# Kernel optimization log

Measured on AMD Instinct MI355X. Metric: run time of the kernel, lower is better.

The kernel has to match this reference:

```python
import jax, jax.numpy as jnp
import numpy as np

B, T, D, H, E, K = 8, 4096, 768, 3072, 4, 2


def setup_inputs() -> dict:
    key = jax.random.key(0)
    ks = jax.random.split(key, 7)
    s = 0.02
    return {
        "x": jax.random.normal(ks[0], (B, T, D), dtype=jnp.float32),
        "router_w": jax.random.normal(ks[1], (D, E), dtype=jnp.float32) * s,
        "router_b": jnp.zeros((E,), dtype=jnp.float32),
        "W1": jax.random.normal(ks[2], (E, D, H), dtype=jnp.float32) * s,
        "b1": jnp.zeros((E, H), dtype=jnp.float32),
        "W2": jax.random.normal(ks[3], (E, H, D), dtype=jnp.float32) * s,
        "b2": jnp.zeros((E, D), dtype=jnp.float32),
    }


def reference(x, router_w, router_b, W1, b1, W2, b2):
    # Router: softmax over experts, then top-k selection.
    logits = jnp.einsum('btd,de->bte', x, router_w) + router_b        # [B,T,E]
    probs = jax.nn.softmax(logits, axis=-1)                           # [B,T,E]
    topk_probs, topk_idx = jax.lax.top_k(probs, K)                    # [B,T,K]

    # Per-expert combine weight: sum of top-k probs assigned to expert e.
    onehot = jax.nn.one_hot(topk_idx, E, dtype=x.dtype)               # [B,T,K,E]
    w = jnp.einsum('btk,btke->bte', topk_probs, onehot)               # [B,T,E]

    # Expert FFNs (exact-erf GELU matches torch F.gelu default).
    out = jnp.zeros_like(x)
    for e in range(E):
        h = jax.nn.gelu(jnp.einsum('btd,dh->bth', x, W1[e]) + b1[e], approximate=False)
        y = jnp.einsum('bth,hd->btd', h, W2[e]) + b2[e]
        out = out + w[..., e:e + 1] * y

    # Load-balance loss: expert assignment counts (non-differentiable, from int idx).
    counts = onehot.sum(axis=(0, 1, 2))                               # [E]
    token_fraction = counts / counts.sum()
    router_prob_mean = probs.mean(axis=(0, 1))                        # [E]
    load_balance_loss = E * jnp.sum(router_prob_mean * token_fraction)
    return out, load_balance_loss
```

## Files before the change

### kernel.cpp

```cpp
#include <hip/hip_runtime.h>
#include <hip/hip_bf16.h>
#include <hip/hip_fp16.h>

#define N_TOK 32768
#define D_DIM 768
#define H_DIM 3072
#define E_NUM 4
#define MT_PAD (N_TOK + 512)

#define TILE_E 4096

typedef _Float16 f16_t;
typedef _Float16 f16x8 __attribute__((ext_vector_type(8)));
typedef float f32x4 __attribute__((ext_vector_type(4)));

__device__ __forceinline__ f16_t f2h(float f) { return (f16_t)f; }

__device__ __forceinline__ void gload16(const void* g, void* l) {
  __builtin_amdgcn_global_load_lds(
      (const __attribute__((address_space(1))) void*)g,
      (__attribute__((address_space(3))) void*)l,
      16, 0, 0);
}

__device__ __forceinline__ void pipe_barrier() {
  asm volatile("" ::: "memory");
  __builtin_amdgcn_sched_barrier(0);
  __builtin_amdgcn_s_barrier();
  __builtin_amdgcn_sched_barrier(0);
  asm volatile("" ::: "memory");
}

__device__ __forceinline__ int xcd_swizzle(int f, int nwg) {
  const int q = nwg >> 3, r = nwg & 7;
  const int xcd = f & 7, pos = f >> 3;
  return (xcd < r ? xcd * (q + 1) : r * (q + 1) + (xcd - r) * q) + pos;
}


__global__ __launch_bounds__(256) void fill_kernel(unsigned* __restrict__ idx0,
                                                   unsigned* __restrict__ idx1) {
  const int t = blockIdx.x * 256 + threadIdx.x;
  for (int i = t; i < MT_PAD; i += gridDim.x * 256) {
    idx0[i] = 0xFFFFFFFFu;
    idx1[i] = 0xFFFFFFFFu;
  }
}

__global__ __launch_bounds__(256) void transform_kernel(
    const float* __restrict__ in, f16_t* __restrict__ outT,
    int R, int C, int NT, int KT) {
  __shared__ float tile[32][33];
  const int ez = blockIdx.z;
  in += (size_t)ez * R * C;
  const int c0 = blockIdx.x * 32, r0 = blockIdx.y * 32;
  const int tc = threadIdx.x & 31, tr = threadIdx.x >> 5;
#pragma unroll
  for (int i = 0; i < 32; i += 8)
    tile[tr + i][tc] = in[(size_t)(r0 + tr + i) * C + c0 + tc];
  __syncthreads();
  const int kt = r0 >> 5, g = tc >> 3, kk = tc & 7;
#pragma unroll
  for (int i = 0; i < 32; i += 8) {
    const int n = c0 + tr + i;
    const int nt = n >> 7, rl = n & 127;
    outT[(((size_t)(ez * NT + nt)) * KT + kt) * TILE_E + g * 1024 + rl * 8 + kk]
        = f2h(tile[tc][tr + i]);
  }
}

__global__ __launch_bounds__(256) void router_kernel(
    const float* __restrict__ x, const float* __restrict__ rw, const float* __restrict__ rb,
    float* __restrict__ wcomb, int* __restrict__ pairinfo,
    float* __restrict__ psum_part, int* __restrict__ cnt_part,
    int* __restrict__ cnt0_part, int* __restrict__ cnt1_part) {
  __shared__ float rwT[E_NUM][D_DIM];
  __shared__ float prW[4][E_NUM];
  __shared__ int   cnW[4][E_NUM];
  __shared__ int   cn0W[4][E_NUM];
  __shared__ int   cn1W[4][E_NUM];
  const int tid = threadIdx.x;
  for (int i = tid; i < D_DIM * E_NUM; i += 256) {
    int k = i >> 2, e = i & 3;
    rwT[e][k] = rw[i];
  }
  __syncthreads();
  const int lane = tid & 63, wv_ = tid >> 6;
  float pacc[E_NUM] = {0.f, 0.f, 0.f, 0.f};
  int   cacc[E_NUM] = {0, 0, 0, 0};
  int   c0acc[E_NUM] = {0, 0, 0, 0};
  int   c1acc[E_NUM] = {0, 0, 0, 0};
  const int tok0 = blockIdx.x * 32 + wv_ * 8;
  for (int t = 0; t < 8; ++t) {
    const int m = tok0 + t;
    const float* xr = x + (size_t)m * D_DIM;
    float s0 = 0.f, s1 = 0.f, s2 = 0.f, s3 = 0.f;
#pragma unroll
    for (int i = 0; i < D_DIM / 64; ++i) {
      int k = lane + i * 64;
      float xv = xr[k];
      s0 += xv * rwT[0][k]; s1 += xv * rwT[1][k];
      s2 += xv * rwT[2][k]; s3 += xv * rwT[3][k];
    }
#pragma unroll
    for (int off = 32; off >= 1; off >>= 1) {
      s0 += __shfl_xor(s0, off); s1 += __shfl_xor(s1, off);
      s2 += __shfl_xor(s2, off); s3 += __shfl_xor(s3, off);
    }
    if (lane == 0) {
      float lg[4] = {s0 + rb[0], s1 + rb[1], s2 + rb[2], s3 + rb[3]};
      float mx = fmaxf(fmaxf(lg[0], lg[1]), fmaxf(lg[2], lg[3]));
      float p[4]; float den = 0.f;
#pragma unroll
      for (int e = 0; e < 4; ++e) { p[e] = expf(lg[e] - mx); den += p[e]; }
      float inv = 1.f / den;
#pragma unroll
      for (int e = 0; e < 4; ++e) p[e] *= inv;
      int i1 = 0;
#pragma unroll
      for (int e = 1; e < 4; ++e) if (p[e] > p[i1]) i1 = e;
      int i2 = (i1 == 0) ? 1 : 0;
#pragma unroll
      for (int e = 0; e < 4; ++e) if (e != i1 && p[e] > p[i2]) i2 = e;
      float4 wvout;
      wvout.x = (0 == i1 || 0 == i2) ? p[0] : 0.f;
      wvout.y = (1 == i1 || 1 == i2) ? p[1] : 0.f;
      wvout.z = (2 == i1 || 2 == i2) ? p[2] : 0.f;
      wvout.w = (3 == i1 || 3 == i2) ? p[3] : 0.f;
      ((float4*)wcomb)[m] = wvout;
      const int emin = (i1 < i2) ? i1 : i2;
      const int emax = (i1 < i2) ? i2 : i1;
      pairinfo[m] = emin | (emax << 4);
      c0acc[emin]++; c1acc[emax]++;
#pragma unroll
      for (int e = 0; e < 4; ++e) pacc[e] += p[e];
      cacc[i1]++; cacc[i2]++;
    }
  }
  if (lane == 0) {
#pragma unroll
    for (int e = 0; e < 4; ++e) {
      prW[wv_][e] = pacc[e]; cnW[wv_][e] = cacc[e];
      cn0W[wv_][e] = c0acc[e]; cn1W[wv_][e] = c1acc[e];
    }
  }
  __syncthreads();
  if (tid < 4) {
    float ps = prW[0][tid] + prW[1][tid] + prW[2][tid] + prW[3][tid];
    int   cs = cnW[0][tid] + cnW[1][tid] + cnW[2][tid] + cnW[3][tid];
    psum_part[blockIdx.x * 4 + tid] = ps;
    cnt_part[blockIdx.x * 4 + tid]  = cs;
    cnt0_part[blockIdx.x * 4 + tid] = cn0W[0][tid] + cn0W[1][tid] + cn0W[2][tid] + cn0W[3][tid];
    cnt1_part[blockIdx.x * 4 + tid] = cn1W[0][tid] + cn1W[1][tid] + cn1W[2][tid] + cn1W[3][tid];
  }
}

__global__ void loss_kernel(const float* __restrict__ psum_part,
                            const int* __restrict__ cnt_part,
                            float* __restrict__ loss_out, int nblk) {
  const int lane = threadIdx.x;
  float ps[4] = {0.f, 0.f, 0.f, 0.f};
  int   cs[4] = {0, 0, 0, 0};
  for (int r = lane; r < nblk; r += 64) {
#pragma unroll
    for (int e = 0; e < 4; ++e) { ps[e] += psum_part[r * 4 + e]; cs[e] += cnt_part[r * 4 + e]; }
  }
#pragma unroll
  for (int off = 32; off >= 1; off >>= 1) {
#pragma unroll
    for (int e = 0; e < 4; ++e) {
      ps[e] += __shfl_xor(ps[e], off);
      cs[e] += __shfl_xor(cs[e], off);
    }
  }
  if (lane == 0) {
    float loss = 0.f;
#pragma unroll
    for (int e = 0; e < 4; ++e) {
      float mean = ps[e] / (float)N_TOK;
      float frac = (float)cs[e] / (float)(N_TOK * 2);
      loss += mean * frac;
    }
    loss_out[0] = 4.f * loss;
  }
}

__global__ __launch_bounds__(256) void setup_kernel(const int* __restrict__ cnt0_part,
                                                    const int* __restrict__ cnt1_part,
                                                    int* __restrict__ meta, int nblk) {
  __shared__ int sh[8][32];
  const int ch = threadIdx.x >> 5, ln = threadIdx.x & 31;
  const int* src = (ch < 4) ? cnt0_part : cnt1_part;
  const int e = ch & 3;
  int s = 0;
  for (int b = ln; b < nblk; b += 32) s += src[b * 4 + e];
  sh[ch][ln] = s;
  __syncthreads();
  if (threadIdx.x == 0) {
    int c[8];
    for (int c2 = 0; c2 < 8; ++c2) {
      int t = 0;
      for (int l = 0; l < 32; ++l) t += sh[c2][l];
      c[c2] = t;
    }
    int pb = 0; meta[8] = 0;
    for (int e2 = 0; e2 < 4; ++e2) { pb += (c[e2] + 127) & ~127; meta[9 + e2] = pb; }
    pb = 0; meta[13] = 0;
    for (int e2 = 0; e2 < 4; ++e2) { pb += (c[4 + e2] + 127) & ~127; meta[14 + e2] = pb; }
    for (int e2 = 0; e2 < 4; ++e2) { meta[18 + e2] = meta[8 + e2]; meta[22 + e2] = meta[13 + e2]; }
  }
}

__global__ __launch_bounds__(256) void scatter_kernel(const int* __restrict__ pairinfo,
                                                      int* __restrict__ meta,
                                                      unsigned* __restrict__ idx0,
                                                      unsigned* __restrict__ idx1) {
  __shared__ int wcnt[2][4][4];
  __shared__ int blkbase[2][4];
  const int tid = threadIdx.x, lane = tid & 63, wv = tid >> 6;
  const int t = blockIdx.x * 256 + tid;
  const int info = pairinfo[t];
  const int esel0 = info & 15, esel1 = info >> 4;
  int rank0 = 0, rank1 = 0;
#pragma unroll
  for (int e = 0; e < 4; ++e) {
    unsigned long long m0 = __ballot(esel0 == e);
    if (esel0 == e) rank0 = __popcll(m0 & ((1ull << lane) - 1ull));
    unsigned long long m1 = __ballot(esel1 == e);
    if (esel1 == e) rank1 = __popcll(m1 & ((1ull << lane) - 1ull));
    if (lane == 0) { wcnt[0][wv][e] = __popcll(m0); wcnt[1][wv][e] = __popcll(m1); }
  }
  __syncthreads();
  int wbase0 = 0, wbase1 = 0;
  for (int w = 0; w < wv; ++w) { wbase0 += wcnt[0][w][esel0]; wbase1 += wcnt[1][w][esel1]; }
  if (tid < 8) {
    const int p = tid >> 2, e = tid & 3;
    const int tot = wcnt[p][0][e] + wcnt[p][1][e] + wcnt[p][2][e] + wcnt[p][3][e];
    blkbase[p][e] = atomicAdd(&meta[(p ? 22 : 18) + e], tot);
  }
  __syncthreads();
  idx0[blkbase[0][esel0] + wbase0 + rank0] = (unsigned)t;
  idx1[blkbase[1][esel1] + wbase1 + rank1] = (unsigned)t;
}

__global__ __launch_bounds__(256) void gather_kernel(
    const float* __restrict__ x, const unsigned* __restrict__ idx_p,
    f16_t* __restrict__ xg, int srow) {
  __shared__ unsigned idx_s[128];
  const int tid = threadIdx.x, mt = blockIdx.x;
  if (tid < 128) {
    const int gr = srow + mt * 128 + tid;
    idx_s[tid] = (gr < MT_PAD) ? idx_p[gr] : 0xFFFFFFFFu;
  }
  __syncthreads();
  f16_t* dst = xg + (size_t)mt * 24 * TILE_E;
  for (int i = tid; i < 128 * 96; i += 256) {
    const int r = i / 96, grp = i - r * 96;
    const unsigned v = idx_s[r];
    const float* src = x + (size_t)((v < N_TOK) ? v : 0u) * D_DIM + grp * 8;
    float4 f0 = ((const float4*)src)[0];
    float4 f1 = ((const float4*)src)[1];
    f16x8 h;
    h[0] = f2h(f0.x); h[1] = f2h(f0.y); h[2] = f2h(f0.z); h[3] = f2h(f0.w);
    h[4] = f2h(f1.x); h[5] = f2h(f1.y); h[6] = f2h(f1.z); h[7] = f2h(f1.w);
    const int kt = grp >> 2, g = grp & 3;
    *(f16x8*)&dst[(size_t)kt * TILE_E + g * 1024 + r * 8] = h;
  }
}

#define BM 128
#define BN 128

#define MFMA_HALF(AvBase, BvBase)                                                   \
  {                                                                                 \
    const f16x8* Av = (const f16x8*)(AvBase);                                       \
    const f16x8* Bv = (const f16x8*)(BvBase);                                       \
    const int gsel = (lane >> 4) * 128;                                             \
    f16x8 a[4], b[4];                                                               \
    _Pragma("unroll")                                                               \
    for (int mf = 0; mf < 4; ++mf) a[mf] = Av[gsel + wr * 64 + mf * 16 + (lane & 15)]; \
    _Pragma("unroll")                                                               \
    for (int nf = 0; nf < 4; ++nf) b[nf] = Bv[gsel + wc * 64 + nf * 16 + (lane & 15)]; \
    _Pragma("unroll")                                                               \
    for (int mf = 0; mf < 4; ++mf)                                                  \
      _Pragma("unroll")                                                             \
      for (int nf = 0; nf < 4; ++nf)                                                \
        acc[mf][nf] = __builtin_amdgcn_mfma_f32_16x16x32_f16(a[mf], b[nf], acc[mf][nf], 0, 0, 0); \
  }

__global__ __launch_bounds__(256, 3) void gemm1_kernel(
    const f16_t* __restrict__ xg, const f16_t* __restrict__ W1T,
    const float* __restrict__ b1, const int* __restrict__ pb_p,
    f16_t* __restrict__ HwP, int srow) {
  __shared__ __align__(16) f16_t As[2 * TILE_E];
  __shared__ __align__(16) f16_t Bs[2 * TILE_E];
  const int tid = threadIdx.x, lane = tid & 63, wid = tid >> 6;
  const int wg = xcd_swizzle(blockIdx.x, gridDim.x);
  const int ntile = wg % 24, mtile = wg / 24;
  const int m128 = srow + mtile * BM;
  if (m128 >= pb_p[4]) return;
  int e = 0;
  while (e < 3 && m128 >= pb_p[e + 1]) ++e;
  const int n0 = ntile * BN;

  const f16_t* abase = xg + (size_t)mtile * 24 * TILE_E + lane * 8;
  const f16_t* bbase = W1T + (size_t)(e * 24 + ntile) * 24 * TILE_E + lane * 8;

  auto stage = [&](int kt, int h) {
    const f16_t* a = abase + (size_t)kt * TILE_E;
    const f16_t* b = bbase + (size_t)kt * TILE_E;
    gload16(a + wid * 512,        &As[h * TILE_E + wid * 512]);
    gload16(a + 2048 + wid * 512, &As[h * TILE_E + 2048 + wid * 512]);
    gload16(b + wid * 512,        &Bs[h * TILE_E + wid * 512]);
    gload16(b + 2048 + wid * 512, &Bs[h * TILE_E + 2048 + wid * 512]);
  };

  const int wr = wid >> 1, wc = wid & 1;
  f32x4 acc[4][4] = {};

  float b1v[4];
#pragma unroll
  for (int nf = 0; nf < 4; ++nf)
    b1v[nf] = b1[e * H_DIM + n0 + wc * 64 + nf * 16 + (lane & 15)];

  const int NT2 = (D_DIM / 32) / 2;
  for (int t = 0; t < NT2; ++t) {
    stage(2 * t, 0);
    stage(2 * t + 1, 1);
    __syncthreads();
    MFMA_HALF(As, Bs);
    MFMA_HALF(As + TILE_E, Bs + TILE_E);
    __syncthreads();
  }

  const int colb = wc * 64 + (lane & 15);
#pragma unroll
  for (int mf = 0; mf < 4; ++mf) {
    const int rowb = wr * 64 + mf * 16 + ((lane >> 4) << 2);
#pragma unroll
    for (int nf = 0; nf < 4; ++nf) {
      const int col = n0 + colb + nf * 16;
      const int kt = col >> 5, g = (col >> 3) & 3, kk = col & 7;
#pragma unroll
      for (int j = 0; j < 4; ++j) {
        const int row = rowb + j;
        float v = acc[mf][nf][j] + b1v[nf];
        float gel = 0.5f * v * (1.0f + erff(v * 0.70710678118654752440f));
        HwP[((size_t)(mtile * 96 + kt)) * TILE_E + g * 1024 + row * 8 + kk] = f2h(gel);
      }
    }
  }
}

__global__ __launch_bounds__(256, 3) void gemm2_kernel(
    const f16_t* __restrict__ HwP, const f16_t* __restrict__ W2T,
    const float* __restrict__ b2, const float* __restrict__ wcomb,
    const unsigned* __restrict__ idx_p, const int* __restrict__ pb_p,
    float* __restrict__ out, int srow, int doAdd) {
  __shared__ __align__(16) f16_t As[3][TILE_E];
  __shared__ __align__(16) f16_t Bs[3][TILE_E];
  __shared__ unsigned idx_s[BM];
  __shared__ float w_s[BM];
  const int tid = threadIdx.x, lane = tid & 63, wid = tid >> 6;
  const int wg = xcd_swizzle(blockIdx.x, gridDim.x);
  const int ntile = wg % 6, mtile = wg / 6;
  const int m128 = srow + mtile * BM;
  if (m128 >= pb_p[4]) return;
  int e = 0;
  while (e < 3 && m128 >= pb_p[e + 1]) ++e;
  const int n0 = ntile * BN;

  if (tid < BM) idx_s[tid] = idx_p[m128 + tid];
  __syncthreads();
  if (tid < BM) {
    unsigned v = idx_s[tid];
    w_s[tid] = (v < N_TOK) ? wcomb[v * 4 + e] : 0.f;
  }

  const f16_t* abase = HwP + (size_t)mtile * 96 * TILE_E + lane * 8;
  const f16_t* bbase = W2T + (size_t)(e * 6 + ntile) * 96 * TILE_E + lane * 8;

  auto stage = [&](int kt, int buf) {
    const f16_t* a = abase + (size_t)kt * TILE_E;
    const f16_t* b = bbase + (size_t)kt * TILE_E;
    gload16(a + wid * 512,        &As[buf][wid * 512]);
    gload16(a + 2048 + wid * 512, &As[buf][2048 + wid * 512]);
    gload16(b + wid * 512,        &Bs[buf][wid * 512]);
    gload16(b + 2048 + wid * 512, &Bs[buf][2048 + wid * 512]);
  };

  const int wr = wid >> 1, wc = wid & 1;
  f32x4 acc[4][4] = {};

  float b2v[4];
#pragma unroll
  for (int nf = 0; nf < 4; ++nf)
    b2v[nf] = b2[e * D_DIM + n0 + wc * 64 + nf * 16 + (lane & 15)];

  stage(0, 0);
  stage(1, 1);
  const int NT = H_DIM / 32;
  int cur = 0;
  for (int t = 0; t < NT; ++t) {
    if (t + 1 < NT) { asm volatile("s_waitcnt vmcnt(4)" ::: "memory"); }
    else            { asm volatile("s_waitcnt vmcnt(0)" ::: "memory"); }
    pipe_barrier();
    if (t + 2 < NT) stage(t + 2, (t + 2) % 3);
    MFMA_HALF(As[cur], Bs[cur]);
    cur = (cur == 2) ? 0 : cur + 1;
  }

  const int colb = wc * 64 + (lane & 15);
#pragma unroll
  for (int mf = 0; mf < 4; ++mf) {
    const int rowb = wr * 64 + mf * 16 + ((lane >> 4) << 2);
#pragma unroll
    for (int nf = 0; nf < 4; ++nf) {
      const int col = n0 + colb + nf * 16;
#pragma unroll
      for (int j = 0; j < 4; ++j) {
        const int row = rowb + j;
        const unsigned v = idx_s[row];
        if (v < N_TOK) {
          float contrib = w_s[row] * (acc[mf][nf][j] + b2v[nf]);
          float* po = out + (size_t)v * D_DIM + col;
          if (doAdd) *po += contrib; else *po = contrib;
        }
      }
    }
  }
}

extern "C" void kernel_launch(void* const* d_in, const int* in_sizes, int n_in,
                              void* d_out, int out_size, void* d_ws, size_t ws_size,
                              hipStream_t stream) {
  const float* x  = (const float*)d_in[0];
  const float* rw = (const float*)d_in[1];
  const float* rb = (const float*)d_in[2];
  const float* W1 = (const float*)d_in[3];
  const float* b1 = (const float*)d_in[4];
  const float* W2 = (const float*)d_in[5];
  const float* b2 = (const float*)d_in[6];
  float* out = (float*)d_out;

  char* ws = (char*)d_ws;
  size_t off = 0;
  auto alloc = [&](size_t bytes) -> void* {
    void* p = ws + off;
    off = (off + bytes + 255) & ~(size_t)255;
    return p;
  };
  f16_t* W1T = (f16_t*)alloc((size_t)E_NUM * D_DIM * H_DIM * sizeof(f16_t));
  f16_t* W2T = (f16_t*)alloc((size_t)E_NUM * D_DIM * H_DIM * sizeof(f16_t));
  float* wcomb = (float*)alloc((size_t)N_TOK * E_NUM * sizeof(float));
  float* psum_part = (float*)alloc((size_t)(N_TOK / 32) * 4 * sizeof(float));
  int*   cnt_part  = (int*)alloc((size_t)(N_TOK / 32) * 4 * sizeof(int));
  int*   cnt0_part = (int*)alloc((size_t)(N_TOK / 32) * 4 * sizeof(int));
  int*   cnt1_part = (int*)alloc((size_t)(N_TOK / 32) * 4 * sizeof(int));
  int*   pairinfo  = (int*)alloc((size_t)N_TOK * sizeof(int));
  int*   meta      = (int*)alloc(32 * sizeof(int));
  unsigned* idx0   = (unsigned*)alloc((size_t)MT_PAD * sizeof(unsigned));
  unsigned* idx1   = (unsigned*)alloc((size_t)MT_PAD * sizeof(unsigned));

  size_t avail = (ws_size > off) ? ws_size - off : 0;
  int hwrows = (int)(avail / 7680);
  if (hwrows > MT_PAD) hwrows = MT_PAD;
  hwrows &= ~127;
  if (hwrows < 128) hwrows = 128;
  const int chunks = (MT_PAD + hwrows - 1) / hwrows;
  f16_t* xg  = (f16_t*)(ws + off);
  f16_t* HwP = (f16_t*)(ws + off + (size_t)hwrows * D_DIM * sizeof(f16_t));

  const int nblk = N_TOK / 32;

  fill_kernel<<<128, 256, 0, stream>>>(idx0, idx1);
  transform_kernel<<<dim3(H_DIM / 32, D_DIM / 32, E_NUM), 256, 0, stream>>>(W1, W1T, D_DIM, H_DIM, 24, 24);
  transform_kernel<<<dim3(D_DIM / 32, H_DIM / 32, E_NUM), 256, 0, stream>>>(W2, W2T, H_DIM, D_DIM, 6, 96);
  router_kernel<<<nblk, 256, 0, stream>>>(x, rw, rb, wcomb, pairinfo,
                                          psum_part, cnt_part, cnt0_part, cnt1_part);
  loss_kernel<<<1, 64, 0, stream>>>(psum_part, cnt_part, out + (size_t)N_TOK * D_DIM, nblk);
  setup_kernel<<<1, 256, 0, stream>>>(cnt0_part, cnt1_part, meta, nblk);
  scatter_kernel<<<N_TOK / 256, 256, 0, stream>>>(pairinfo, meta, idx0, idx1);

  for (int pass = 0; pass < 2; ++pass) {
    const unsigned* ip = pass ? idx1 : idx0;
    const int* pbp = meta + (pass ? 13 : 8);
    for (int c = 0; c < chunks; ++c) {
      const int srow = c * hwrows;
      gather_kernel<<<hwrows / 128, 256, 0, stream>>>(x, ip, xg, srow);
      gemm1_kernel<<<(hwrows / 128) * 24, 256, 0, stream>>>(xg, W1T, b1, pbp, HwP, srow);
      gemm2_kernel<<<(hwrows / 128) * 6, 256, 0, stream>>>(HwP, W2T, b2, wcomb, ip, pbp, out, srow, pass);
    }
  }
}
```

Baseline: 1.235 ms.

## Enlarge GEMM tiles to 256x256 with 512-thread blocks and double buffering

```diff
diff --git a/kernel.cpp b/kernel.cpp
--- a/kernel.cpp
+++ b/kernel.cpp
@@ -6,7 +6,7 @@
 #define D_DIM 768
 #define H_DIM 3072
 #define E_NUM 4
-#define MT_PAD (N_TOK + 512)
+#define MT_PAD (N_TOK + 1024)
 
 #define TILE_E 4096
 
@@ -204,9 +204,9 @@
       c[c2] = t;
     }
     int pb = 0; meta[8] = 0;
-    for (int e2 = 0; e2 < 4; ++e2) { pb += (c[e2] + 127) & ~127; meta[9 + e2] = pb; }
+    for (int e2 = 0; e2 < 4; ++e2) { pb += (c[e2] + 255) & ~255; meta[9 + e2] = pb; }
     pb = 0; meta[13] = 0;
-    for (int e2 = 0; e2 < 4; ++e2) { pb += (c[4 + e2] + 127) & ~127; meta[14 + e2] = pb; }
+    for (int e2 = 0; e2 < 4; ++e2) { pb += (c[4 + e2] + 255) & ~255; meta[14 + e2] = pb; }
     for (int e2 = 0; e2 < 4; ++e2) { meta[18 + e2] = meta[8 + e2]; meta[22 + e2] = meta[13 + e2]; }
   }
 }
@@ -268,161 +268,169 @@
   }
 }
 
-#define BM 128
-#define BN 128
-
-#define MFMA_HALF(AvBase, BvBase)                                                   \
-  {                                                                                 \
-    const f16x8* Av = (const f16x8*)(AvBase);                                       \
-    const f16x8* Bv = (const f16x8*)(BvBase);                                       \
-    const int gsel = (lane >> 4) * 128;                                             \
-    f16x8 a[4], b[4];                                                               \
-    _Pragma("unroll")                                                               \
-    for (int mf = 0; mf < 4; ++mf) a[mf] = Av[gsel + wr * 64 + mf * 16 + (lane & 15)]; \
-    _Pragma("unroll")                                                               \
-    for (int nf = 0; nf < 4; ++nf) b[nf] = Bv[gsel + wc * 64 + nf * 16 + (lane & 15)]; \
-    _Pragma("unroll")                                                               \
-    for (int mf = 0; mf < 4; ++mf)                                                  \
-      _Pragma("unroll")                                                             \
-      for (int nf = 0; nf < 4; ++nf)                                                \
-        acc[mf][nf] = __builtin_amdgcn_mfma_f32_16x16x32_f16(a[mf], b[nf], acc[mf][nf], 0, 0, 0); \
-  }
-
-__global__ __launch_bounds__(256, 3) void gemm1_kernel(
+
+#define MFMA_QUAD()                                                               \
+  {                                                                               \
+    const int gsel = (lane >> 4) * 128, l15 = lane & 15;                          \
+    _Pragma("unroll")                                                             \
+    for (int h = 0; h < 2; ++h) {                                                 \
+      const f16x8* Av = (const f16x8*)As[d][wr * 2 + h];                          \
+      const f16x8* Bv = (const f16x8*)Bs[d][(wc >> 1) * 2 + h];                   \
+      f16x8 a[8], b[4];                                                           \
+      _Pragma("unroll")                                                           \
+      for (int mf = 0; mf < 8; ++mf) a[mf] = Av[gsel + mf * 16 + l15];            \
+      _Pragma("unroll")                                                           \
+      for (int nf = 0; nf < 4; ++nf) b[nf] = Bv[gsel + (wc & 1) * 64 + nf * 16 + l15]; \
+      _Pragma("unroll")                                                           \
+      for (int mf = 0; mf < 8; ++mf)                                              \
+        _Pragma("unroll")                                                         \
+        for (int nf = 0; nf < 4; ++nf)                                            \
+          acc[mf][nf] = __builtin_amdgcn_mfma_f32_16x16x32_f16(a[mf], b[nf], acc[mf][nf], 0, 0, 0); \
+    }                                                                             \
+  }
+
+__global__ __launch_bounds__(512, 2) void gemm1_kernel(
     const f16_t* __restrict__ xg, const f16_t* __restrict__ W1T,
     const float* __restrict__ b1, const int* __restrict__ pb_p,
     f16_t* __restrict__ HwP, int srow) {
-  __shared__ __align__(16) f16_t As[2 * TILE_E];
-  __shared__ __align__(16) f16_t Bs[2 * TILE_E];
+  __shared__ __align__(16) f16_t As[2][4][TILE_E];
+  __shared__ __align__(16) f16_t Bs[2][4][TILE_E];
   const int tid = threadIdx.x, lane = tid & 63, wid = tid >> 6;
   const int wg = xcd_swizzle(blockIdx.x, gridDim.x);
-  const int ntile = wg % 24, mtile = wg / 24;
-  const int m128 = srow + mtile * BM;
-  if (m128 >= pb_p[4]) return;
+  const int ntile = wg % 12, mtile = wg / 12;
+  const int m256 = srow + mtile * 256;
+  if (m256 >= pb_p[4]) return;
   int e = 0;
-  while (e < 3 && m128 >= pb_p[e + 1]) ++e;
-  const int n0 = ntile * BN;
-
-  const f16_t* abase = xg + (size_t)mtile * 24 * TILE_E + lane * 8;
-  const f16_t* bbase = W1T + (size_t)(e * 24 + ntile) * 24 * TILE_E + lane * 8;
-
-  auto stage = [&](int kt, int h) {
-    const f16_t* a = abase + (size_t)kt * TILE_E;
-    const f16_t* b = bbase + (size_t)kt * TILE_E;
-    gload16(a + wid * 512,        &As[h * TILE_E + wid * 512]);
-    gload16(a + 2048 + wid * 512, &As[h * TILE_E + 2048 + wid * 512]);
-    gload16(b + wid * 512,        &Bs[h * TILE_E + wid * 512]);
-    gload16(b + 2048 + wid * 512, &Bs[h * TILE_E + 2048 + wid * 512]);
+  while (e < 3 && m256 >= pb_p[e + 1]) ++e;
+  const int n0 = ntile * 256;
+
+  const f16_t* apan0 = xg + (size_t)(2 * mtile + 0) * 24 * TILE_E;
+  const f16_t* apan1 = xg + (size_t)(2 * mtile + 1) * 24 * TILE_E;
+  const f16_t* bpan0 = W1T + (size_t)(e * 24 + 2 * ntile + 0) * 24 * TILE_E;
+  const f16_t* bpan1 = W1T + (size_t)(e * 24 + 2 * ntile + 1) * 24 * TILE_E;
+  const int soff = wid * 512 + lane * 8;
+
+  auto stage = [&](int t, int dd) {
+    const size_t k0 = (size_t)(2 * t) * TILE_E, k1 = k0 + TILE_E;
+    gload16(apan0 + k0 + soff, &As[dd][0][wid * 512]);
+    gload16(apan0 + k1 + soff, &As[dd][1][wid * 512]);
+    gload16(apan1 + k0 + soff, &As[dd][2][wid * 512]);
+    gload16(apan1 + k1 + soff, &As[dd][3][wid * 512]);
+    gload16(bpan0 + k0 + soff, &Bs[dd][0][wid * 512]);
+    gload16(bpan0 + k1 + soff, &Bs[dd][1][wid * 512]);
+    gload16(bpan1 + k0 + soff, &Bs[dd][2][wid * 512]);
+    gload16(bpan1 + k1 + soff, &Bs[dd][3][wid * 512]);
   };
 
-  const int wr = wid >> 1, wc = wid & 1;
-  f32x4 acc[4][4] = {};
+  const int wr = wid >> 2, wc = wid & 3;
+  f32x4 acc[8][4] = {};
 
   float b1v[4];
 #pragma unroll
   for (int nf = 0; nf < 4; ++nf)
     b1v[nf] = b1[e * H_DIM + n0 + wc * 64 + nf * 16 + (lane & 15)];
 
-  const int NT2 = (D_DIM / 32) / 2;
-  for (int t = 0; t < NT2; ++t) {
-    stage(2 * t, 0);
-    stage(2 * t + 1, 1);
-    __syncthreads();
-    MFMA_HALF(As, Bs);
-    MFMA_HALF(As + TILE_E, Bs + TILE_E);
-    __syncthreads();
-  }
-
-  const int colb = wc * 64 + (lane & 15);
-#pragma unroll
-  for (int mf = 0; mf < 4; ++mf) {
-    const int rowb = wr * 64 + mf * 16 + ((lane >> 4) << 2);
+  const int NT = D_DIM / 64;
+  stage(0, 0);
+  for (int t = 0; t < NT; ++t) {
+    const int d = t & 1;
+    asm volatile("s_waitcnt vmcnt(0)" ::: "memory");
+    pipe_barrier();
+    if (t + 1 < NT) stage(t + 1, d ^ 1);
+    MFMA_QUAD();
+  }
+
+#pragma unroll
+  for (int mf = 0; mf < 8; ++mf) {
+    const int row = wr * 128 + mf * 16 + ((lane >> 4) << 2);
+    const int rp = 2 * mtile + (row >> 7), rl = row & 127;
 #pragma unroll
     for (int nf = 0; nf < 4; ++nf) {
-      const int col = n0 + colb + nf * 16;
+      const int col = n0 + wc * 64 + nf * 16 + (lane & 15);
       const int kt = col >> 5, g = (col >> 3) & 3, kk = col & 7;
 #pragma unroll
       for (int j = 0; j < 4; ++j) {
-        const int row = rowb + j;
         float v = acc[mf][nf][j] + b1v[nf];
         float gel = 0.5f * v * (1.0f + erff(v * 0.70710678118654752440f));
-        HwP[((size_t)(mtile * 96 + kt)) * TILE_E + g * 1024 + row * 8 + kk] = f2h(gel);
+        HwP[((size_t)(rp * 96 + kt)) * TILE_E + g * 1024 + (rl + j) * 8 + kk] = f2h(gel);
       }
     }
   }
 }
 
-__global__ __launch_bounds__(256, 3) void gemm2_kernel(
+__global__ __launch_bounds__(512, 2) void gemm2_kernel(
     const f16_t* __restrict__ HwP, const f16_t* __restrict__ W2T,
     const float* __restrict__ b2, const float* __restrict__ wcomb,
     const unsigned* __restrict__ idx_p, const int* __restrict__ pb_p,
     float* __restrict__ out, int srow, int doAdd) {
-  __shared__ __align__(16) f16_t As[3][TILE_E];
-  __shared__ __align__(16) f16_t Bs[3][TILE_E];
-  __shared__ unsigned idx_s[BM];
-  __shared__ float w_s[BM];
+  __shared__ __align__(16) f16_t As[2][4][TILE_E];
+  __shared__ __align__(16) f16_t Bs[2][4][TILE_E];
+  __shared__ unsigned idx_s[256];
+  __shared__ float w_s[256];
   const int tid = threadIdx.x, lane = tid & 63, wid = tid >> 6;
   const int wg = xcd_swizzle(blockIdx.x, gridDim.x);
-  const int ntile = wg % 6, mtile = wg / 6;
-  const int m128 = srow + mtile * BM;
-  if (m128 >= pb_p[4]) return;
+  const int ntile = wg % 3, mtile = wg / 3;
+  const int m256 = srow + mtile * 256;
+  if (m256 >= pb_p[4]) return;
   int e = 0;
-  while (e < 3 && m128 >= pb_p[e + 1]) ++e;
-  const int n0 = ntile * BN;
-
-  if (tid < BM) idx_s[tid] = idx_p[m128 + tid];
-  __syncthreads();
-  if (tid < BM) {
+  while (e < 3 && m256 >= pb_p[e + 1]) ++e;
+  const int n0 = ntile * 256;
+
+  if (tid < 256) idx_s[tid] = idx_p[m256 + tid];
+  __syncthreads();
+  if (tid < 256) {
     unsigned v = idx_s[tid];
     w_s[tid] = (v < N_TOK) ? wcomb[v * 4 + e] : 0.f;
   }
-
-  const f16_t* abase = HwP + (size_t)mtile * 96 * TILE_E + lane * 8;
-  const f16_t* bbase = W2T + (size_t)(e * 6 + ntile) * 96 * TILE_E + lane * 8;
-
-  auto stage = [&](int kt, int buf) {
-    const f16_t* a = abase + (size_t)kt * TILE_E;
-    const f16_t* b = bbase + (size_t)kt * TILE_E;
-    gload16(a + wid * 512,        &As[buf][wid * 512]);
-    gload16(a + 2048 + wid * 512, &As[buf][2048 + wid * 512]);
-    gload16(b + wid * 512,        &Bs[buf][wid * 512]);
-    gload16(b + 2048 + wid * 512, &Bs[buf][2048 + wid * 512]);
+  __syncthreads();
+
+  const f16_t* apan0 = HwP + (size_t)(2 * mtile + 0) * 96 * TILE_E;
+  const f16_t* apan1 = HwP + (size_t)(2 * mtile + 1) * 96 * TILE_E;
+  const f16_t* bpan0 = W2T + (size_t)(e * 6 + 2 * ntile + 0) * 96 * TILE_E;
+  const f16_t* bpan1 = W2T + (size_t)(e * 6 + 2 * ntile + 1) * 96 * TILE_E;
+  const int soff = wid * 512 + lane * 8;
+
+  auto stage = [&](int t, int dd) {
+    const size_t k0 = (size_t)(2 * t) * TILE_E, k1 = k0 + TILE_E;
+    gload16(apan0 + k0 + soff, &As[dd][0][wid * 512]);
+    gload16(apan0 + k1 + soff, &As[dd][1][wid * 512]);
+    gload16(apan1 + k0 + soff, &As[dd][2][wid * 512]);
+    gload16(apan1 + k1 + soff, &As[dd][3][wid * 512]);
+    gload16(bpan0 + k0 + soff, &Bs[dd][0][wid * 512]);
+    gload16(bpan0 + k1 + soff, &Bs[dd][1][wid * 512]);
+    gload16(bpan1 + k0 + soff, &Bs[dd][2][wid * 512]);
+    gload16(bpan1 + k1 + soff, &Bs[dd][3][wid * 512]);
   };
 
-  const int wr = wid >> 1, wc = wid & 1;
-  f32x4 acc[4][4] = {};
+  const int wr = wid >> 2, wc = wid & 3;
+  f32x4 acc[8][4] = {};
 
   float b2v[4];
 #pragma unroll
   for (int nf = 0; nf < 4; ++nf)
     b2v[nf] = b2[e * D_DIM + n0 + wc * 64 + nf * 16 + (lane & 15)];
 
+  const int NT = H_DIM / 64;
   stage(0, 0);
-  stage(1, 1);
-  const int NT = H_DIM / 32;
-  int cur = 0;
   for (int t = 0; t < NT; ++t) {
-    if (t + 1 < NT) { asm volatile("s_waitcnt vmcnt(4)" ::: "memory"); }
-    else            { asm volatile("s_waitcnt vmcnt(0)" ::: "memory"); }
+    const int d = t & 1;
+    asm volatile("s_waitcnt vmcnt(0)" ::: "memory");
     pipe_barrier();
-    if (t + 2 < NT) stage(t + 2, (t + 2) % 3);
-    MFMA_HALF(As[cur], Bs[cur]);
-    cur = (cur == 2) ? 0 : cur + 1;
-  }
-
-  const int colb = wc * 64 + (lane & 15);
-#pragma unroll
-  for (int mf = 0; mf < 4; ++mf) {
-    const int rowb = wr * 64 + mf * 16 + ((lane >> 4) << 2);
+    if (t + 1 < NT) stage(t + 1, d ^ 1);
+    MFMA_QUAD();
+  }
+
+#pragma unroll
+  for (int mf = 0; mf < 8; ++mf) {
+    const int row = wr * 128 + mf * 16 + ((lane >> 4) << 2);
 #pragma unroll
     for (int nf = 0; nf < 4; ++nf) {
-      const int col = n0 + colb + nf * 16;
+      const int col = n0 + wc * 64 + nf * 16 + (lane & 15);
 #pragma unroll
       for (int j = 0; j < 4; ++j) {
-        const int row = rowb + j;
-        const unsigned v = idx_s[row];
+        const unsigned v = idx_s[row + j];
         if (v < N_TOK) {
-          float contrib = w_s[row] * (acc[mf][nf][j] + b2v[nf]);
+          float contrib = w_s[row + j] * (acc[mf][nf][j] + b2v[nf]);
           float* po = out + (size_t)v * D_DIM + col;
           if (doAdd) *po += contrib; else *po = contrib;
         }
@@ -465,9 +473,10 @@
   size_t avail = (ws_size > off) ? ws_size - off : 0;
   int hwrows = (int)(avail / 7680);
   if (hwrows > MT_PAD) hwrows = MT_PAD;
-  hwrows &= ~127;
-  if (hwrows < 128) hwrows = 128;
-  const int chunks = (MT_PAD + hwrows - 1) / hwrows;
+  hwrows &= ~255;
+  if (hwrows < 256) hwrows = 256;
+  int chunks = (MT_PAD + hwrows - 1) / hwrows;
+  hwrows = (((MT_PAD + chunks - 1) / chunks) + 255) & ~255;
   f16_t* xg  = (f16_t*)(ws + off);
   f16_t* HwP = (f16_t*)(ws + off + (size_t)hwrows * D_DIM * sizeof(f16_t));
 
@@ -488,8 +497,8 @@
     for (int c = 0; c < chunks; ++c) {
       const int srow = c * hwrows;
       gather_kernel<<<hwrows / 128, 256, 0, stream>>>(x, ip, xg, srow);
-      gemm1_kernel<<<(hwrows / 128) * 24, 256, 0, stream>>>(xg, W1T, b1, pbp, HwP, srow);
-      gemm2_kernel<<<(hwrows / 128) * 6, 256, 0, stream>>>(HwP, W2T, b2, wcomb, ip, pbp, out, srow, pass);
-    }
-  }
-}
+      gemm1_kernel<<<(hwrows / 256) * 12, 512, 0, stream>>>(xg, W1T, b1, pbp, HwP, srow);
+      gemm2_kernel<<<(hwrows / 256) * 3, 512, 0, stream>>>(HwP, W2T, b2, wcomb, ip, pbp, out, srow, pass);
+    }
+  }
+}
```

Measured after the change: 1.398 ms. +13.2%, slower.
